# Kernel tuning notes

Measured on AMD Instinct MI355X. Metric: run time of the kernel, lower is better.

Reference implementation:

```python
import math
import jax, jax.numpy as jnp
import numpy as np
from jax import lax

# (new_dilation, init_dilation) per layer for layers=3, blocks=2, kernel_size=2
DILATIONS = [(1, 1), (2, 1), (4, 2), (1, 4), (2, 1), (4, 2)]
K = 2  # kernel_size


def dilate(x, dilation, init_dilation):
    """Faithful port of the pad+permute+view+permute trick. x: (n, c, l)."""
    n, c, l = x.shape
    f = dilation / init_dilation
    if f == 1:
        return x
    new_l = int(math.ceil(l / f) * f)
    if new_l != l:
        x = jnp.pad(x, ((0, 0), (0, 0), (new_l - l, 0)))  # pad_start=True
        l = new_l
    l_new = int(math.ceil(l * init_dilation / dilation))
    n_new = int(math.ceil(n * dilation / init_dilation))
    x = jnp.transpose(x, (1, 2, 0)).reshape(c, l_new, n_new)
    return jnp.transpose(x, (2, 0, 1))


def conv2(x, w):
    """1D conv, kernel_size=2, no bias. x:(n,i,l), w:(o,i,2) -> (n,o,l-1)."""
    return (jnp.einsum('oi,nil->nol', w[:, :, 0], x[:, :, :-1])
            + jnp.einsum('oi,nil->nol', w[:, :, 1], x[:, :, 1:]))


def conv1x1(x, w):
    return jnp.einsum('oi,nil->nol', w, x)


def maxpool3s2(x):
    return lax.reduce_window(x, -jnp.inf, lax.max, (1, 1, 3), (1, 1, 2), 'VALID')


def wavenet_logits(x, start_w, filter_w, gate_w, res_w, skip_w,
                   end1_w, end1_b, end2_w, end2_b,
                   fc_w1, fc_b1, fc_w2, fc_b2, fc_w3, fc_b3):
    h = conv1x1(x, start_w)
    skip = None
    for i, (d, idil) in enumerate(DILATIONS):
        residual = dilate(h, d, idil)
        filt = jnp.tanh(conv2(residual, filter_w[i]))
        gate = jax.nn.sigmoid(conv2(residual, gate_w[i]))
        h = filt * gate
        s = h if h.shape[2] == 1 else dilate(h, 1, d)
        s = conv1x1(s, skip_w[i])
        if skip is None:
            skip = s
        else:
            skip = s + skip[:, :, -s.shape[2]:]
        h = conv1x1(h, res_w[i]) + residual[:, :, K - 1:]
    y = jax.nn.relu(skip)                                   # (B, 256, 1272)
    y = jax.nn.relu(conv1x1(y, end1_w) + end1_b[None, :, None])
    y = maxpool3s2(y)                                       # (B, 128, 635)
    y = jax.nn.relu(conv1x1(y, end2_w) + end2_b[None, :, None])
    y = maxpool3s2(y)                                       # (B, 32, 317)
    y = y.reshape(y.shape[0], -1)                           # (B, 10144)
    # output_layer MLP (dropout = identity in eval)
    y = jax.nn.relu(y @ fc_w1.T + fc_b1)
    y = jax.nn.relu(y @ fc_w2.T + fc_b2)
    return y @ fc_w3.T + fc_b3                              # (B, num_classes)


def setup_inputs() -> dict:
    key = jax.random.key(0)
    ks = jax.random.split(key, 12)
    f32 = jnp.float32

    def w(k, shape, fan_in):
        return jax.random.normal(k, shape, f32) / np.sqrt(fan_in).astype(np.float32)

    B, Cin, L = 256, 5, 1280
    return {
        'x': jax.random.normal(ks[0], (B, Cin, L), f32),
        'start_w': w(ks[1], (32, 5), 5),
        'filter_w': w(ks[2], (6, 32, 32, 2), 64),
        'gate_w': w(ks[3], (6, 32, 32, 2), 64),
        'res_w': w(ks[4], (6, 32, 32), 32),
        'skip_w': w(ks[5], (6, 256, 32), 32),
        'end1_w': w(ks[6], (128, 256), 256), 'end1_b': jnp.zeros((128,), f32),
        'end2_w': w(ks[7], (32, 128), 128), 'end2_b': jnp.zeros((32,), f32),
        'fc_w1': w(ks[8], (1024, 10144), 10144), 'fc_b1': jnp.zeros((1024,), f32),
        'fc_w2': w(ks[9], (256, 1024), 1024), 'fc_b2': jnp.zeros((256,), f32),
        'fc_w3': w(ks[10], (2, 256), 256), 'fc_b3': jnp.zeros((2,), f32),
    }


def reference(x, start_w, filter_w, gate_w, res_w, skip_w,
              end1_w, end1_b, end2_w, end2_b,
              fc_w1, fc_b1, fc_w2, fc_b2, fc_w3, fc_b3):
    logits = wavenet_logits(x, start_w, filter_w, gate_w, res_w, skip_w,
                            end1_w, end1_b, end2_w, end2_b,
                            fc_w1, fc_b1, fc_w2, fc_b2, fc_w3, fc_b3)
    y_prob = jax.nn.softmax(logits, axis=1)
    y_hat = jnp.argmax(logits, axis=1)
    return logits, y_prob, y_hat
```

## Files before the change

### kernel.cpp

```cpp
#include <hip/hip_runtime.h>
#include <math.h>


#define MCAP 327680

typedef short v8s __attribute__((ext_vector_type(8)));
typedef float v4f __attribute__((ext_vector_type(4)));

static inline long lmax_(long a, long b) { return a > b ? a : b; }

__device__ inline unsigned short rnbf(float x) {
    unsigned u = __float_as_uint(x);
    return (unsigned short)((u + 0x7FFFu + ((u >> 16) & 1u)) >> 16);
}
__device__ inline void split2(float v, unsigned short& h, unsigned short& l) {
    h = rnbf(v);
    const float hf = __uint_as_float(((unsigned)h) << 16);
    l = rnbf(v - hf);
}
__device__ inline unsigned packsplit(float v) {
    unsigned short h, l;
    split2(v, h, l);
    return ((unsigned)l << 16) | (unsigned)h;
}
__device__ inline float unpack2f(unsigned v) {
    return __uint_as_float(v << 16) + __uint_as_float(v & 0xffff0000u);
}

__global__ __launch_bounds__(256) void k_zero(float* __restrict__ p, int n) {
    int i = blockIdx.x * 256 + threadIdx.x;
    if (i < n) p[i] = 0.f;
}

__global__ __launch_bounds__(256) void k_start(const float* __restrict__ x,
                                               const float* __restrict__ sw,
                                               unsigned* __restrict__ h0) {
    int j = blockIdx.x * 256 + threadIdx.x;
    int t = j >> 8, n = j & 255;
    float xv[5];
#pragma unroll
    for (int i = 0; i < 5; ++i) xv[i] = x[n * 6400 + i * 1280 + t];
#pragma unroll
    for (int o = 0; o < 32; ++o) {
        float acc = 0.f;
#pragma unroll
        for (int i = 0; i < 5; ++i) acc = fmaf(sw[o * 5 + i], xv[i], acc);
        h0[o * MCAP + j] = packsplit(acc);
    }
}

__global__ __launch_bounds__(256) void k_prep(const float* __restrict__ skw,
                                              const float* __restrict__ e1w,
                                              const float* __restrict__ fw,
                                              const float* __restrict__ gw,
                                              const float* __restrict__ rw,
                                              const float* __restrict__ e2w,
                                              unsigned short* __restrict__ swt_hi,
                                              unsigned short* __restrict__ swt_lo,
                                              unsigned short* __restrict__ e1t_hi,
                                              unsigned short* __restrict__ e1t_lo,
                                              unsigned short* __restrict__ wfg_hi,
                                              unsigned short* __restrict__ wfg_lo,
                                              unsigned short* __restrict__ wr_hi,
                                              unsigned short* __restrict__ wr_lo,
                                              unsigned short* __restrict__ e2s_hi,
                                              unsigned short* __restrict__ e2s_lo) {
    int idx = blockIdx.x * 256 + threadIdx.x;
    if (idx < 49152) {
        int ch = idx / 192, k = idx - ch * 192;
        int l = k >> 5, i = k & 31;
        unsigned short h, lo;
        split2(skw[l * 8192 + ch * 32 + i], h, lo);
        swt_hi[idx] = h; swt_lo[idx] = lo;
    }
    if (idx < 32768) {
        unsigned short h, lo;
        split2(e1w[idx], h, lo);
        e1t_hi[idx] = h; e1t_lo[idx] = lo;
    }
    if (idx < 24576) {
        int l = idx >> 12, r = idx & 4095;
        int row = r >> 6, k = r & 63;
        int o = row & 31, i = k & 31, tap = k >> 5;
        const float* src = (row < 32) ? fw : gw;
        unsigned short h, lo;
        split2(src[l * 2048 + o * 64 + i * 2 + tap], h, lo);
        wfg_hi[idx] = h; wfg_lo[idx] = lo;
    }
    if (idx < 12288) {
        int l = idx >> 11, r = idx & 2047;
        int o = r >> 6, k = r & 63, i = k & 31;
        unsigned short h, lo;
        split2(rw[l * 1024 + o * 32 + i], h, lo);
        wr_hi[idx] = h; wr_lo[idx] = lo;
    }
    if (idx < 4096) {
        unsigned short h, lo;
        split2(e2w[idx], h, lo);
        e2s_hi[idx] = h; e2s_lo[idx] = lo;
    }
}

__global__ __launch_bounds__(256) void k_prep_w1(const float* __restrict__ w1,
                                                 unsigned short* __restrict__ hi,
                                                 unsigned short* __restrict__ lo) {
    int idx = blockIdx.x * 256 + threadIdx.x;
    if (idx < 10387456) {
        unsigned short h, l;
        split2(w1[idx], h, l);
        hi[idx] = h; lo[idx] = l;
    }
}

__global__ __launch_bounds__(256) void k_layer_m(
    const unsigned* __restrict__ hin, const int hinBase, const int hinStride,
    unsigned* __restrict__ hout, const int houtBase, const int houtStride,
    unsigned* __restrict__ gsl, const int gStride,
    const unsigned short* __restrict__ wfg_hi, const unsigned short* __restrict__ wfg_lo,
    const unsigned short* __restrict__ wr_hi, const unsigned short* __restrict__ wr_lo,
    const int Jlo, const int NpmP, const int padN,
    const int so_, const int M0, const int M1, const int doRes)
{
    __shared__ unsigned short U[128 * 136];
    unsigned short* AT = U;
    unsigned short* GT = U;

    const int tid = threadIdx.x;
    const int j0 = Jlo + blockIdx.x * 128;

    {
        const int col = tid & 127;
        const int kg = tid >> 7;
        unsigned short* bh = &AT[col * 136 + kg * 32];
        unsigned short* bl = &AT[col * 136 + 64 + kg * 32];
        if (kg == 0 && j0 < padN) {
            uint4 z; z.x = z.y = z.z = z.w = 0u;
#pragma unroll
            for (int ch = 0; ch < 32; ch += 8) {
                *(uint4*)&bh[ch] = z;
                *(uint4*)&bl[ch] = z;
            }
        } else {
            const int off = (kg == 0) ? (j0 - padN) : (j0 + NpmP);
            const unsigned* p = hin + (off - hinBase) + col;
#pragma unroll
            for (int ch = 0; ch < 32; ch += 8) {
                alignas(16) unsigned short h8[8], l8[8];
#pragma unroll
                for (int u = 0; u < 8; ++u) {
                    const unsigned v = p[(size_t)(ch + u) * hinStride];
                    h8[u] = (unsigned short)(v & 0xffffu);
                    l8[u] = (unsigned short)(v >> 16);
                }
                *(uint4*)&bh[ch] = *(uint4*)h8;
                *(uint4*)&bl[ch] = *(uint4*)l8;
            }
        }
    }
    __syncthreads();

    const int lane = tid & 63;
    const int w    = tid >> 6;
    const int ch2  = w >> 1;
    const int mh   = w & 1;
    const int l15  = lane & 15;
    const int quad = lane >> 4;
    const int q8   = quad * 8;
    const int colb = ch2 * 64;

    v4f accf[4], accg[4];
#pragma unroll
    for (int nt = 0; nt < 4; ++nt) { accf[nt] = (v4f)(0.f); accg[nt] = (v4f)(0.f); }

#pragma unroll
    for (int kt = 0; kt < 2; ++kt) {
        const int frow = (mh * 16 + l15) * 64 + kt * 32 + q8;
        const int grow = (32 + mh * 16 + l15) * 64 + kt * 32 + q8;
        const v8s afh = *(const v8s*)&wfg_hi[frow];
        const v8s afl = *(const v8s*)&wfg_lo[frow];
        const v8s agh = *(const v8s*)&wfg_hi[grow];
        const v8s agl = *(const v8s*)&wfg_lo[grow];
#pragma unroll
        for (int nt = 0; nt < 4; ++nt) {
            const int col = colb + nt * 16 + l15;
            const v8s bh = *(const v8s*)&AT[col * 136 + kt * 32 + q8];
            const v8s bl = *(const v8s*)&AT[col * 136 + 64 + kt * 32 + q8];
            accf[nt] = __builtin_amdgcn_mfma_f32_16x16x32_bf16(afh, bh, accf[nt], 0, 0, 0);
            accf[nt] = __builtin_amdgcn_mfma_f32_16x16x32_bf16(afh, bl, accf[nt], 0, 0, 0);
            accf[nt] = __builtin_amdgcn_mfma_f32_16x16x32_bf16(afl, bh, accf[nt], 0, 0, 0);
            accg[nt] = __builtin_amdgcn_mfma_f32_16x16x32_bf16(agh, bh, accg[nt], 0, 0, 0);
            accg[nt] = __builtin_amdgcn_mfma_f32_16x16x32_bf16(agh, bl, accg[nt], 0, 0, 0);
            accg[nt] = __builtin_amdgcn_mfma_f32_16x16x32_bf16(agl, bh, accg[nt], 0, 0, 0);
        }
    }

    unsigned short gh[4][4], gl[4][4];
#pragma unroll
    for (int nt = 0; nt < 4; ++nt)
#pragma unroll
        for (int r = 0; r < 4; ++r) {
            const float f = accf[nt][r];
            const float g = accg[nt][r];
            const float th = 1.f - 2.f / (__expf(2.f * f) + 1.f);
            const float sg = 1.f / (1.f + __expf(-g));
            split2(th * sg, gh[nt][r], gl[nt][r]);
        }

    const int m0c = j0 - so_;
    if (m0c >= M0 && m0c < M1) {
#pragma unroll
        for (int nt = 0; nt < 4; ++nt)
#pragma unroll
            for (int r = 0; r < 4; ++r) {
                const int ch = mh * 16 + quad * 4 + r;
                const int m = (m0c - M0) + colb + nt * 16 + l15;
                gsl[(size_t)ch * gStride + m] =
                    ((unsigned)gl[nt][r] << 16) | (unsigned)gh[nt][r];
            }
    }

    if (doRes) {
        __syncthreads();
#pragma unroll
        for (int nt = 0; nt < 4; ++nt)
#pragma unroll
            for (int r = 0; r < 4; ++r) {
                const int ch = mh * 16 + quad * 4 + r;
                const int col = colb + nt * 16 + l15;
                GT[col * 72 + ch] = gh[nt][r];
                GT[col * 72 + 32 + ch] = gl[nt][r];
            }
        __syncthreads();

        v4f accr[4];
#pragma unroll
        for (int nt = 0; nt < 4; ++nt) accr[nt] = (v4f)(0.f);
#pragma unroll
        for (int kt = 0; kt < 2; ++kt) {
            const int row = (mh * 16 + l15) * 64 + kt * 32 + q8;
            const v8s arh = *(const v8s*)&wr_hi[row];
            const v8s arl = *(const v8s*)&wr_lo[row];
#pragma unroll
            for (int nt = 0; nt < 4; ++nt) {
                const int col = colb + nt * 16 + l15;
                const v8s b = *(const v8s*)&GT[col * 72 + kt * 32 + q8];
                accr[nt] = __builtin_amdgcn_mfma_f32_16x16x32_bf16(arh, b, accr[nt], 0, 0, 0);
                accr[nt] = __builtin_amdgcn_mfma_f32_16x16x32_bf16(arl, b, accr[nt], 0, 0, 0);
            }
        }

        const unsigned* tp = hin + (j0 + NpmP - hinBase);
#pragma unroll
        for (int nt = 0; nt < 4; ++nt)
#pragma unroll
            for (int r = 0; r < 4; ++r) {
                const int o = mh * 16 + quad * 4 + r;
                const int col = colb + nt * 16 + l15;
                const float tap1 = unpack2f(tp[(size_t)o * hinStride + col]);
                hout[(size_t)o * houtStride + (j0 - houtBase) + col] =
                    packsplit(accr[nt][r] + tap1);
            }
    }
}

__global__ __launch_bounds__(256, 2) void k_skip_end1_m(
    const unsigned* __restrict__ g,
    const unsigned short* __restrict__ swt_hi, const unsigned short* __restrict__ swt_lo,
    const unsigned short* __restrict__ e1t_hi, const unsigned short* __restrict__ e1t_lo,
    const float* __restrict__ b1, float* __restrict__ y1, const int gs)
{
    __shared__ unsigned short U[33792];
    unsigned short* gt_hi = U;
    unsigned short* gt_lo = U + 12800;
    unsigned short* st_hi = U;
    unsigned short* st_lo = U + 16896;

    const int tid  = threadIdx.x;
    const int m0   = blockIdx.x * 64;
    const int lane = tid & 63;
    const int w    = tid >> 6;
    const int l15  = lane & 15;
    const int q8   = (lane >> 4) * 8;
    const int rbase = (lane >> 4) * 4;

    {
        const int scol = tid & 63;
        const int ks0  = (tid >> 6) * 8;
        for (int kc = 0; kc < 192; kc += 32) {
            alignas(16) unsigned short h8[8], l8[8];
#pragma unroll
            for (int j = 0; j < 8; ++j) {
                const int k = kc + ks0 + j;
                const unsigned v = g[(size_t)(k >> 5) * 32 * gs + (size_t)(k & 31) * gs + m0 + scol];
                h8[j] = (unsigned short)(v & 0xffffu);
                l8[j] = (unsigned short)(v >> 16);
            }
            *(v8s*)&gt_hi[scol * 200 + kc + ks0] = *(v8s*)h8;
            *(v8s*)&gt_lo[scol * 200 + kc + ks0] = *(v8s*)l8;
        }
    }
    __syncthreads();

    v4f acc1[4][4];
#pragma unroll
    for (int a = 0; a < 4; ++a)
#pragma unroll
        for (int b = 0; b < 4; ++b) acc1[a][b] = (v4f)(0.f);

    for (int kc = 0; kc < 192; kc += 32) {
        v8s ah[4], al[4], bh[4], bl[4];
#pragma unroll
        for (int t = 0; t < 4; ++t) {
            const int row = (w * 64 + t * 16 + l15) * 192 + kc + q8;
            ah[t] = *(const v8s*)&swt_hi[row];
            al[t] = *(const v8s*)&swt_lo[row];
            const int bo = (t * 16 + l15) * 200 + kc + q8;
            bh[t] = *(const v8s*)&gt_hi[bo];
            bl[t] = *(const v8s*)&gt_lo[bo];
        }
#pragma unroll
        for (int ct = 0; ct < 4; ++ct)
#pragma unroll
            for (int nt = 0; nt < 4; ++nt) {
                acc1[ct][nt] = __builtin_amdgcn_mfma_f32_16x16x32_bf16(ah[ct], bh[nt], acc1[ct][nt], 0, 0, 0);
                acc1[ct][nt] = __builtin_amdgcn_mfma_f32_16x16x32_bf16(ah[ct], bl[nt], acc1[ct][nt], 0, 0, 0);
                acc1[ct][nt] = __builtin_amdgcn_mfma_f32_16x16x32_bf16(al[ct], bh[nt], acc1[ct][nt], 0, 0, 0);
            }
    }
    __syncthreads();

#pragma unroll
    for (int ct = 0; ct < 4; ++ct)
#pragma unroll
        for (int nt = 0; nt < 4; ++nt) {
            alignas(8) unsigned short sh[4], sl[4];
#pragma unroll
            for (int r = 0; r < 4; ++r) {
                const float v = fmaxf(acc1[ct][nt][r], 0.f);
                split2(v, sh[r], sl[r]);
            }
            const int ci  = w * 64 + ct * 16 + rbase;
            const int col = nt * 16 + l15;
            *(uint2*)&st_hi[col * 264 + ci] = *(uint2*)sh;
            *(uint2*)&st_lo[col * 264 + ci] = *(uint2*)sl;
        }
    __syncthreads();

    v4f acc2[2][4];
#pragma unroll
    for (int a = 0; a < 2; ++a)
#pragma unroll
        for (int b = 0; b < 4; ++b) acc2[a][b] = (v4f)(0.f);

    for (int kc = 0; kc < 256; kc += 32) {
        v8s ah[2], al[2], bh[4], bl[4];
#pragma unroll
        for (int t = 0; t < 2; ++t) {
            const int row = (w * 32 + t * 16 + l15) * 256 + kc + q8;
            ah[t] = *(const v8s*)&e1t_hi[row];
            al[t] = *(const v8s*)&e1t_lo[row];
        }
#pragma unroll
        for (int t = 0; t < 4; ++t) {
            const int bo = (t * 16 + l15) * 264 + kc + q8;
            bh[t] = *(const v8s*)&st_hi[bo];
            bl[t] = *(const v8s*)&st_lo[bo];
        }
#pragma unroll
        for (int ct = 0; ct < 2; ++ct)
#pragma unroll
            for (int nt = 0; nt < 4; ++nt) {
                acc2[ct][nt] = __builtin_amdgcn_mfma_f32_16x16x32_bf16(ah[ct], bh[nt], acc2[ct][nt], 0, 0, 0);
                acc2[ct][nt] = __builtin_amdgcn_mfma_f32_16x16x32_bf16(ah[ct], bl[nt], acc2[ct][nt], 0, 0, 0);
                acc2[ct][nt] = __builtin_amdgcn_mfma_f32_16x16x32_bf16(al[ct], bh[nt], acc2[ct][nt], 0, 0, 0);
            }
    }

#pragma unroll
    for (int ct = 0; ct < 2; ++ct) {
        const int cobase = w * 32 + ct * 16 + rbase;
        float bb[4];
#pragma unroll
        for (int r = 0; r < 4; ++r) bb[r] = b1[cobase + r];
#pragma unroll
        for (int nt = 0; nt < 4; ++nt) {
            const int col = m0 + nt * 16 + l15;
#pragma unroll
            for (int r = 0; r < 4; ++r)
                y1[(size_t)(cobase + r) * gs + col] = fmaxf(acc2[ct][nt][r] + bb[r], 0.f);
        }
    }
}

__global__ __launch_bounds__(256) void k_pe2_m(
    const float* __restrict__ y1c,
    const unsigned short* __restrict__ e2s_hi, const unsigned short* __restrict__ e2s_lo,
    const float* __restrict__ b2, float* __restrict__ e2c,
    const int gs, const int p1s)
{
    __shared__ unsigned short SP[2 * 64 * 136];
    unsigned short* sp_hi = SP;
    unsigned short* sp_lo = SP + 64 * 136;

    const int tid = threadIdx.x;
    const int m0 = blockIdx.x * 64;
    const int tp = m0 >> 8;
    const int nb = m0 & 255;

    {
        const int col = tid & 63;
        const int cig = tid >> 6;
        const int base = 2 * tp * 256 + nb + col;
#pragma unroll
        for (int u8 = 0; u8 < 4; ++u8) {
            alignas(16) unsigned short h8[8], l8[8];
#pragma unroll
            for (int u = 0; u < 8; ++u) {
                const int ci = cig * 32 + u8 * 8 + u;
                const float* yp = y1c + (size_t)ci * gs + base;
                const float v = fmaxf(fmaxf(yp[0], yp[256]), yp[512]);
                split2(v, h8[u], l8[u]);
            }
            *(uint4*)&sp_hi[col * 136 + cig * 32 + u8 * 8] = *(uint4*)h8;
            *(uint4*)&sp_lo[col * 136 + cig * 32 + u8 * 8] = *(uint4*)l8;
        }
    }
    __syncthreads();

    const int lane = tid & 63;
    const int w    = tid >> 6;
    const int mh   = w & 1;
    const int colh = w >> 1;
    const int l15  = lane & 15;
    const int quad = lane >> 4;
    const int q8   = quad * 8;

    v4f acc[2];
    acc[0] = (v4f)(0.f); acc[1] = (v4f)(0.f);

#pragma unroll
    for (int kc = 0; kc < 128; kc += 32) {
        const int row = (mh * 16 + l15) * 128 + kc + q8;
        const v8s ah = *(const v8s*)&e2s_hi[row];
        const v8s al = *(const v8s*)&e2s_lo[row];
#pragma unroll
        for (int nt = 0; nt < 2; ++nt) {
            const int col = colh * 32 + nt * 16 + l15;
            const v8s bh = *(const v8s*)&sp_hi[col * 136 + kc + q8];
            const v8s bl = *(const v8s*)&sp_lo[col * 136 + kc + q8];
            acc[nt] = __builtin_amdgcn_mfma_f32_16x16x32_bf16(ah, bh, acc[nt], 0, 0, 0);
            acc[nt] = __builtin_amdgcn_mfma_f32_16x16x32_bf16(ah, bl, acc[nt], 0, 0, 0);
            acc[nt] = __builtin_amdgcn_mfma_f32_16x16x32_bf16(al, bh, acc[nt], 0, 0, 0);
        }
    }

#pragma unroll
    for (int nt = 0; nt < 2; ++nt)
#pragma unroll
        for (int r = 0; r < 4; ++r) {
            const int co = mh * 16 + quad * 4 + r;
            const int col = m0 + colh * 32 + nt * 16 + l15;
            e2c[(size_t)co * p1s + col] = fmaxf(acc[nt][r] + b2[co], 0.f);
        }
}

__global__ __launch_bounds__(256) void k_pool2p(const float* __restrict__ e2c,
                                                unsigned* __restrict__ p2,
                                                const int p1s, const int A) {
    const int n = threadIdx.x, tl2 = blockIdx.x, co = blockIdx.y;
    const int base = co * p1s + tl2 * 512 + n;
    float v = fmaxf(fmaxf(e2c[base], e2c[base + 256]), e2c[base + 512]);
    p2[co * 81152 + (A + tl2) * 256 + n] = packsplit(v);
}

__global__ __launch_bounds__(256) void k_fc1_m(
    const unsigned short* __restrict__ w1s_hi, const unsigned short* __restrict__ w1s_lo,
    const unsigned* __restrict__ p2u, float* __restrict__ out)
{
    __shared__ unsigned short SB[2 * 64 * 40];
    unsigned short* sb_hi = SB;
    unsigned short* sb_lo = SB + 64 * 40;

    const int tid = threadIdx.x;
    const int o0 = blockIdx.x * 64;
    const int b0 = blockIdx.y * 64;
    const int k0 = blockIdx.z * 1280;
    const int kend = (k0 + 1280 < 10144) ? (k0 + 1280) : 10144;
    const int nch = (kend - k0) >> 5;

    const int lane = tid & 63;
    const int w    = tid >> 6;
    const int l15  = lane & 15;
    const int quad = lane >> 4;
    const int q8   = quad * 8;
    const int scol = tid & 63;
    const int kq   = tid >> 6;

    v4f acc[4];
#pragma unroll
    for (int nt = 0; nt < 4; ++nt) acc[nt] = (v4f)(0.f);

    for (int c = 0; c < nch; ++c) {
        const int kc = k0 + c * 32;
        alignas(16) unsigned short h8[8], l8[8];
#pragma unroll
        for (int j = 0; j < 8; ++j) {
            const unsigned v = p2u[(size_t)(kc + kq * 8 + j) * 256 + b0 + scol];
            h8[j] = (unsigned short)(v & 0xffffu);
            l8[j] = (unsigned short)(v >> 16);
        }
        __syncthreads();
        *(v8s*)&sb_hi[scol * 40 + kq * 8] = *(v8s*)h8;
        *(v8s*)&sb_lo[scol * 40 + kq * 8] = *(v8s*)l8;
        __syncthreads();

        const int arow = (o0 + w * 16 + l15) * 10144 + kc + q8;
        const v8s ah = *(const v8s*)&w1s_hi[arow];
        const v8s al = *(const v8s*)&w1s_lo[arow];
#pragma unroll
        for (int nt = 0; nt < 4; ++nt) {
            const v8s bh = *(const v8s*)&sb_hi[(nt * 16 + l15) * 40 + q8];
            const v8s bl = *(const v8s*)&sb_lo[(nt * 16 + l15) * 40 + q8];
            acc[nt] = __builtin_amdgcn_mfma_f32_16x16x32_bf16(ah, bh, acc[nt], 0, 0, 0);
            acc[nt] = __builtin_amdgcn_mfma_f32_16x16x32_bf16(ah, bl, acc[nt], 0, 0, 0);
            acc[nt] = __builtin_amdgcn_mfma_f32_16x16x32_bf16(al, bh, acc[nt], 0, 0, 0);
        }
    }

#pragma unroll
    for (int nt = 0; nt < 4; ++nt)
#pragma unroll
        for (int r = 0; r < 4; ++r)
            atomicAdd(&out[(size_t)(o0 + w * 16 + quad * 4 + r) * 256 + b0 + nt * 16 + l15],
                      acc[nt][r]);
}

__global__ __launch_bounds__(256) void k_gemm64(const float* __restrict__ A,
                                                const float* __restrict__ B,
                                                float* __restrict__ C,
                                                const int Ktot, const int KC) {
    __shared__ float sA[32 * 65];
    __shared__ float sB[32 * 68];

    const int tid = threadIdx.x;
    const int o0 = blockIdx.x * 64;
    const int b0 = blockIdx.y * 64;
    const int k0 = blockIdx.z * KC;

    float acc[4][4];
#pragma unroll
    for (int i = 0; i < 4; ++i)
#pragma unroll
        for (int jq = 0; jq < 4; ++jq) acc[i][jq] = 0.f;

    const int ao  = tid >> 2;
    const int ak8 = (tid & 3) * 8;
    const int bk  = tid >> 3;
    const int bb8 = (tid & 7) * 8;
    const int to4 = (tid & 15) * 4;
    const int tb4 = (tid >> 4) * 4;

    for (int kc = 0; kc < KC; kc += 32) {
        const int kcLen = (KC - kc < 32) ? (KC - kc) : 32;
        const float* ap = A + (size_t)(o0 + ao) * Ktot + k0 + kc + ak8;
#pragma unroll
        for (int i = 0; i < 8; ++i) {
            float v = (ak8 + i < kcLen) ? ap[i] : 0.f;
            sA[(ak8 + i) * 65 + ao] = v;
        }
        if (bk < kcLen) {
            const float* bp = B + (size_t)(k0 + kc + bk) * 256 + b0 + bb8;
            const float4 v0 = *(const float4*)bp;
            const float4 v1 = *(const float4*)(bp + 4);
            *(float4*)&sB[bk * 68 + bb8] = v0;
            *(float4*)&sB[bk * 68 + bb8 + 4] = v1;
        } else {
            float4 z; z.x = z.y = z.z = z.w = 0.f;
            *(float4*)&sB[bk * 68 + bb8] = z;
            *(float4*)&sB[bk * 68 + bb8 + 4] = z;
        }
        __syncthreads();

#pragma unroll 8
        for (int kk = 0; kk < 32; ++kk) {
            const float4 av = *(const float4*)&sA[kk * 65 + to4];
            const float4 bv = *(const float4*)&sB[kk * 68 + tb4];
            const float aa[4] = {av.x, av.y, av.z, av.w};
#pragma unroll
            for (int i = 0; i < 4; ++i) {
                acc[i][0] = fmaf(aa[i], bv.x, acc[i][0]);
                acc[i][1] = fmaf(aa[i], bv.y, acc[i][1]);
                acc[i][2] = fmaf(aa[i], bv.z, acc[i][2]);
                acc[i][3] = fmaf(aa[i], bv.w, acc[i][3]);
            }
        }
        __syncthreads();
    }

#pragma unroll
    for (int i = 0; i < 4; ++i)
#pragma unroll
        for (int jq = 0; jq < 4; ++jq)
            atomicAdd(&C[(size_t)(o0 + to4 + i) * 256 + b0 + tb4 + jq], acc[i][jq]);
}

__global__ __launch_bounds__(256) void k_actbias(const float* __restrict__ raw,
                                                 const float* __restrict__ bias,
                                                 float* __restrict__ out) {
    const int k = blockIdx.x, b = threadIdx.x;
    out[k * 256 + b] = fmaxf(raw[k * 256 + b] + bias[k], 0.f);
}

__global__ __launch_bounds__(256) void k_fc3(const float* __restrict__ fc2raw,
                                             const float* __restrict__ fb2,
                                             const float* __restrict__ w3,
                                             const float* __restrict__ b3,
                                             float* __restrict__ out) {
    const int b = threadIdx.x;
    float l0 = b3[0], l1 = b3[1];
    for (int k = 0; k < 256; ++k) {
        const float a = fmaxf(fc2raw[k * 256 + b] + fb2[k], 0.f);
        l0 = fmaf(w3[k], a, l0);
        l1 = fmaf(w3[256 + k], a, l1);
    }
    out[2 * b] = l0;
    out[2 * b + 1] = l1;
    const float mx = fmaxf(l0, l1);
    const float e0 = expf(l0 - mx), e1 = expf(l1 - mx);
    const float inv = 1.f / (e0 + e1);
    out[512 + 2 * b] = e0 * inv;
    out[513 + 2 * b] = e1 * inv;
    out[1024 + b] = (l1 > l0) ? 1.f : 0.f;
}

extern "C" void kernel_launch(void* const* d_in, const int* in_sizes, int n_in,
                              void* d_out, int out_size, void* d_ws, size_t ws_size,
                              hipStream_t stream) {
    const float* x        = (const float*)d_in[0];
    const float* start_w  = (const float*)d_in[1];
    const float* filter_w = (const float*)d_in[2];
    const float* gate_w   = (const float*)d_in[3];
    const float* res_w    = (const float*)d_in[4];
    const float* skip_w   = (const float*)d_in[5];
    const float* e1w      = (const float*)d_in[6];
    const float* e1b      = (const float*)d_in[7];
    const float* e2w      = (const float*)d_in[8];
    const float* e2b      = (const float*)d_in[9];
    const float* w1       = (const float*)d_in[10];
    const float* fb1      = (const float*)d_in[11];
    const float* w2       = (const float*)d_in[12];
    const float* fb2      = (const float*)d_in[13];
    const float* w3       = (const float*)d_in[14];
    const float* b3       = (const float*)d_in[15];

    float* ws = (float*)d_ws;

    const long o_h0   = 0;
    const long o_p2   = 10485760;
    const long o_fc1  = 13082624;
    const long o_fc2  = 13344768;
    const long o_wbf  = 13410304;
    const long o_wfg  = 13492224;
    const long o_wr   = 13516800;
    const long o_e2s  = 13529088;
    const long o_act1 = 13533184;
    const long o_w1s  = 13795328;
    const long o_G    = 24182784;

    long budget = (long)((double)ws_size * 0.94 / 4.0);
    int dB = 1;
    for (int d = 317; d >= 1; --d) {
        long mch = 256L * (4L * d + 3), hs = mch + 4096;
        long tot = o_G + 192L * mch + lmax_(128L * mch, 64L * hs);
        if (tot <= budget) { dB = d; break; }
    }
    int K = (317 + dB - 1) / dB;
    dB = (317 + K - 1) / K;
    const long MchA  = 256L * (4L * dB + 3);
    const long HSPAN = MchA + 4096;
    const long o_X   = o_G + 192L * MchA;
    const long P1S   = 256L * (2L * dB + 1);

    unsigned* h0 = (unsigned*)(ws + o_h0);
    unsigned* p2 = (unsigned*)(ws + o_p2);
    float* fc1r = ws + o_fc1;
    float* fc2r = ws + o_fc2;
    unsigned short* swt_hi = (unsigned short*)(ws + o_wbf);
    unsigned short* swt_lo = swt_hi + 49152;
    unsigned short* e1t_hi = swt_lo + 49152;
    unsigned short* e1t_lo = e1t_hi + 32768;
    unsigned short* wfg_hi = (unsigned short*)(ws + o_wfg);
    unsigned short* wfg_lo = wfg_hi + 24576;
    unsigned short* wr_hi  = (unsigned short*)(ws + o_wr);
    unsigned short* wr_lo  = wr_hi + 12288;
    unsigned short* e2s_hi = (unsigned short*)(ws + o_e2s);
    unsigned short* e2s_lo = e2s_hi + 4096;
    unsigned short* w1s_hi = (unsigned short*)(ws + o_w1s);
    unsigned short* w1s_lo = w1s_hi + 10387456;
    float* act1 = ws + o_act1;
    unsigned* G  = (unsigned*)(ws + o_G);
    unsigned* hA = (unsigned*)(ws + o_X);
    unsigned* hB = (unsigned*)(ws + o_X) + 32L * HSPAN;
    float* y1c  = ws + o_X;
    float* e2c  = ws + o_G;

    k_zero<<<1280, 256, 0, stream>>>(fc1r, 327680);
    k_start<<<1280, 256, 0, stream>>>(x, start_w, h0);
    k_prep<<<192, 256, 0, stream>>>(skip_w, e1w, filter_w, gate_w, res_w, e2w,
                                    swt_hi, swt_lo, e1t_hi, e1t_lo,
                                    wfg_hi, wfg_lo, wr_hi, wr_lo,
                                    e2s_hi, e2s_lo);
    k_prep_w1<<<40576, 256, 0, stream>>>(w1, w1s_hi, w1s_lo);

    const int Mc[6]   = {327424, 327168, 326656, 326400, 326144, 325632};
    const int NpmP[6] = {256, 256, 512, 256, 256, 512};
    const int pN[6]   = {0, 256, 512, 0, 256, 512};
    const int so_[6]  = {1792, 1536, 1024, 768, 512, 0};
    const int JloO[6] = {-1536, -1280, -768, -768, -512, 0};

    for (int c = 0; c < K; ++c) {
        const int A = c * dB;
        int B = A + dB; if (B > 317) B = 317;
        const int dBc = B - A;
        const int M0 = 1024 * A;
        int tmax = 4 * B + 3; if (tmax > 1272) tmax = 1272;
        const int Tt = tmax - 4 * A;
        const int M1 = M0 + 256 * Tt;

        int Jlo[6], Jhi[6];
        for (int q = 0; q < 6; ++q) {
            int lo = M0 + JloO[q]; if (lo < 0) lo = 0;
            int hi = M1 + so_[q];  if (hi > Mc[q]) hi = Mc[q];
            Jlo[q] = lo; Jhi[q] = hi;
        }

        for (int q = 0; q < 6; ++q) {
            const unsigned* hin = (q == 0) ? h0 : ((q & 1) ? hA : hB);
            const int hinBase   = (q == 0) ? 0 : Jlo[q - 1];
            const int hinStride = (q == 0) ? MCAP : (int)HSPAN;
            unsigned* hout = (q & 1) ? hB : hA;
            const int Jcnt = Jhi[q] - Jlo[q];
            k_layer_m<<<Jcnt / 128, 256, 0, stream>>>(
                hin, hinBase, hinStride, hout, Jlo[q], (int)HSPAN,
                G + (long)q * 32 * MchA, (int)MchA,
                wfg_hi + q * 4096, wfg_lo + q * 4096,
                wr_hi + q * 2048, wr_lo + q * 2048,
                Jlo[q], NpmP[q], pN[q], so_[q], M0, M1, (q < 5) ? 1 : 0);
        }

        const int Mchc = 256 * Tt;
        k_skip_end1_m<<<Mchc / 64, 256, 0, stream>>>(
            G, swt_hi, swt_lo, e1t_hi, e1t_lo, e1b, y1c, (int)MchA);
        const int T1c = 2 * dBc + 1;
        k_pe2_m<<<T1c * 4, 256, 0, stream>>>(
            y1c, e2s_hi, e2s_lo, e2b, e2c, (int)MchA, (int)P1S);
        k_pool2p<<<dim3(dBc, 32), 256, 0, stream>>>(e2c, p2, (int)P1S, A);
    }

    k_fc1_m<<<dim3(16, 4, 8), 256, 0, stream>>>(w1s_hi, w1s_lo, p2, fc1r);
    k_actbias<<<1024, 256, 0, stream>>>(fc1r, fb1, act1);
    k_gemm64<<<dim3(4, 4, 4), 256, 0, stream>>>(w2, act1, fc2r, 1024, 256);
    k_fc3<<<1, 256, 0, stream>>>(fc2r, fb2, w3, b3, (float*)d_out);
}
```

Before: 836.9 us.

## Halve shared memory in skip/end1 kernel via two-phase K staging for occupancy

The fused skip+end1 kernel now stages the gated input in two K-halves and processes the 256-channel intermediate in two 128-channel halves, cutting LDS from about 66KB to about 34KB. The end1 weights are permuted at prep time so each half's channel ordering matches the new per-wave layout. Launch bounds rise from 2 to 4 blocks per SM to exploit the freed LDS. This trades extra barriers and register pressure (acc1 plus acc2 live at once under a tighter VGPR budget) for higher occupancy.

```diff
diff --git a/kernel.cpp b/kernel.cpp
--- a/kernel.cpp
+++ b/kernel.cpp
@@ -74,8 +74,11 @@
         swt_hi[idx] = h; swt_lo[idx] = lo;
     }
     if (idx < 32768) {
+        int co = idx >> 8, kn = idx & 255;
+        int hf = kn >> 7, wv = (kn >> 5) & 3, c = (kn >> 4) & 1, r = kn & 15;
+        int ch = wv * 64 + (hf * 2 + c) * 16 + r;
         unsigned short h, lo;
-        split2(e1w[idx], h, lo);
+        split2(e1w[co * 256 + ch], h, lo);
         e1t_hi[idx] = h; e1t_lo[idx] = lo;
     }
     if (idx < 24576) {
@@ -263,17 +266,17 @@
     }
 }
 
-__global__ __launch_bounds__(256, 2) void k_skip_end1_m(
+__global__ __launch_bounds__(256, 4) void k_skip_end1_m(
     const unsigned* __restrict__ g,
     const unsigned short* __restrict__ swt_hi, const unsigned short* __restrict__ swt_lo,
     const unsigned short* __restrict__ e1t_hi, const unsigned short* __restrict__ e1t_lo,
     const float* __restrict__ b1, float* __restrict__ y1, const int gs)
 {
-    __shared__ unsigned short U[33792];
+    __shared__ unsigned short U[17408];
     unsigned short* gt_hi = U;
-    unsigned short* gt_lo = U + 12800;
+    unsigned short* gt_lo = U + 6656;
     unsigned short* st_hi = U;
-    unsigned short* st_lo = U + 16896;
+    unsigned short* st_lo = U + 8704;
 
     const int tid  = threadIdx.x;
     const int m0   = blockIdx.x * 64;
@@ -283,97 +286,105 @@
     const int q8   = (lane >> 4) * 8;
     const int rbase = (lane >> 4) * 4;
 
-    {
-        const int scol = tid & 63;
-        const int ks0  = (tid >> 6) * 8;
-        for (int kc = 0; kc < 192; kc += 32) {
+    const int scol = tid & 63;
+    const int ks0  = (tid >> 6) * 8;
+
+    v4f acc1[4][4];
+#pragma unroll
+    for (int a = 0; a < 4; ++a)
+#pragma unroll
+        for (int b = 0; b < 4; ++b) acc1[a][b] = (v4f)(0.f);
+
+#pragma unroll
+    for (int ph = 0; ph < 2; ++ph) {
+        for (int kc = 0; kc < 96; kc += 32) {
             alignas(16) unsigned short h8[8], l8[8];
 #pragma unroll
             for (int j = 0; j < 8; ++j) {
-                const int k = kc + ks0 + j;
+                const int k = ph * 96 + kc + ks0 + j;
                 const unsigned v = g[(size_t)(k >> 5) * 32 * gs + (size_t)(k & 31) * gs + m0 + scol];
                 h8[j] = (unsigned short)(v & 0xffffu);
                 l8[j] = (unsigned short)(v >> 16);
             }
-            *(v8s*)&gt_hi[scol * 200 + kc + ks0] = *(v8s*)h8;
-            *(v8s*)&gt_lo[scol * 200 + kc + ks0] = *(v8s*)l8;
-        }
-    }
-    __syncthreads();
-
-    v4f acc1[4][4];
-#pragma unroll
-    for (int a = 0; a < 4; ++a)
-#pragma unroll
-        for (int b = 0; b < 4; ++b) acc1[a][b] = (v4f)(0.f);
-
-    for (int kc = 0; kc < 192; kc += 32) {
-        v8s ah[4], al[4], bh[4], bl[4];
-#pragma unroll
-        for (int t = 0; t < 4; ++t) {
-            const int row = (w * 64 + t * 16 + l15) * 192 + kc + q8;
-            ah[t] = *(const v8s*)&swt_hi[row];
-            al[t] = *(const v8s*)&swt_lo[row];
-            const int bo = (t * 16 + l15) * 200 + kc + q8;
-            bh[t] = *(const v8s*)&gt_hi[bo];
-            bl[t] = *(const v8s*)&gt_lo[bo];
-        }
-#pragma unroll
-        for (int ct = 0; ct < 4; ++ct)
+            *(v8s*)&gt_hi[scol * 104 + kc + ks0] = *(v8s*)h8;
+            *(v8s*)&gt_lo[scol * 104 + kc + ks0] = *(v8s*)l8;
+        }
+        __syncthreads();
+
+        for (int kc = 0; kc < 96; kc += 32) {
+            v8s ah[4], al[4], bh[4], bl[4];
+#pragma unroll
+            for (int t = 0; t < 4; ++t) {
+                const int row = (w * 64 + t * 16 + l15) * 192 + ph * 96 + kc + q8;
+                ah[t] = *(const v8s*)&swt_hi[row];
+                al[t] = *(const v8s*)&swt_lo[row];
+                const int bo = (t * 16 + l15) * 104 + kc + q8;
+                bh[t] = *(const v8s*)&gt_hi[bo];
+                bl[t] = *(const v8s*)&gt_lo[bo];
+            }
+#pragma unroll
+            for (int ct = 0; ct < 4; ++ct)
+#pragma unroll
+                for (int nt = 0; nt < 4; ++nt) {
+                    acc1[ct][nt] = __builtin_amdgcn_mfma_f32_16x16x32_bf16(ah[ct], bh[nt], acc1[ct][nt], 0, 0, 0);
+                    acc1[ct][nt] = __builtin_amdgcn_mfma_f32_16x16x32_bf16(ah[ct], bl[nt], acc1[ct][nt], 0, 0, 0);
+                    acc1[ct][nt] = __builtin_amdgcn_mfma_f32_16x16x32_bf16(al[ct], bh[nt], acc1[ct][nt], 0, 0, 0);
+                }
+        }
+        __syncthreads();
+    }
+
+    v4f acc2[2][4];
+#pragma unroll
+    for (int a = 0; a < 2; ++a)
+#pragma unroll
+        for (int b = 0; b < 4; ++b) acc2[a][b] = (v4f)(0.f);
+
+#pragma unroll
+    for (int hh = 0; hh < 2; ++hh) {
+#pragma unroll
+        for (int c2 = 0; c2 < 2; ++c2) {
+            const int ct = hh * 2 + c2;
 #pragma unroll
             for (int nt = 0; nt < 4; ++nt) {
-                acc1[ct][nt] = __builtin_amdgcn_mfma_f32_16x16x32_bf16(ah[ct], bh[nt], acc1[ct][nt], 0, 0, 0);
-                acc1[ct][nt] = __builtin_amdgcn_mfma_f32_16x16x32_bf16(ah[ct], bl[nt], acc1[ct][nt], 0, 0, 0);
-                acc1[ct][nt] = __builtin_amdgcn_mfma_f32_16x16x32_bf16(al[ct], bh[nt], acc1[ct][nt], 0, 0, 0);
-            }
-    }
-    __syncthreads();
-
-#pragma unroll
-    for (int ct = 0; ct < 4; ++ct)
-#pragma unroll
-        for (int nt = 0; nt < 4; ++nt) {
-            alignas(8) unsigned short sh[4], sl[4];
-#pragma unroll
-            for (int r = 0; r < 4; ++r) {
-                const float v = fmaxf(acc1[ct][nt][r], 0.f);
-                split2(v, sh[r], sl[r]);
-            }
-            const int ci  = w * 64 + ct * 16 + rbase;
-            const int col = nt * 16 + l15;
-            *(uint2*)&st_hi[col * 264 + ci] = *(uint2*)sh;
-            *(uint2*)&st_lo[col * 264 + ci] = *(uint2*)sl;
-        }
-    __syncthreads();
-
-    v4f acc2[2][4];
-#pragma unroll
-    for (int a = 0; a < 2; ++a)
-#pragma unroll
-        for (int b = 0; b < 4; ++b) acc2[a][b] = (v4f)(0.f);
-
-    for (int kc = 0; kc < 256; kc += 32) {
-        v8s ah[2], al[2], bh[4], bl[4];
-#pragma unroll
-        for (int t = 0; t < 2; ++t) {
-            const int row = (w * 32 + t * 16 + l15) * 256 + kc + q8;
-            ah[t] = *(const v8s*)&e1t_hi[row];
-            al[t] = *(const v8s*)&e1t_lo[row];
-        }
-#pragma unroll
-        for (int t = 0; t < 4; ++t) {
-            const int bo = (t * 16 + l15) * 264 + kc + q8;
-            bh[t] = *(const v8s*)&st_hi[bo];
-            bl[t] = *(const v8s*)&st_lo[bo];
-        }
-#pragma unroll
-        for (int ct = 0; ct < 2; ++ct)
-#pragma unroll
-            for (int nt = 0; nt < 4; ++nt) {
-                acc2[ct][nt] = __builtin_amdgcn_mfma_f32_16x16x32_bf16(ah[ct], bh[nt], acc2[ct][nt], 0, 0, 0);
-                acc2[ct][nt] = __builtin_amdgcn_mfma_f32_16x16x32_bf16(ah[ct], bl[nt], acc2[ct][nt], 0, 0, 0);
-                acc2[ct][nt] = __builtin_amdgcn_mfma_f32_16x16x32_bf16(al[ct], bh[nt], acc2[ct][nt], 0, 0, 0);
-            }
+                alignas(8) unsigned short sh[4], sl[4];
+#pragma unroll
+                for (int r = 0; r < 4; ++r) {
+                    const float v = fmaxf(acc1[ct][nt][r], 0.f);
+                    split2(v, sh[r], sl[r]);
+                }
+                const int ci  = w * 32 + c2 * 16 + rbase;
+                const int col = nt * 16 + l15;
+                *(uint2*)&st_hi[col * 136 + ci] = *(uint2*)sh;
+                *(uint2*)&st_lo[col * 136 + ci] = *(uint2*)sl;
+            }
+        }
+        __syncthreads();
+
+        for (int kc = 0; kc < 128; kc += 32) {
+            v8s ah2[2], al2[2], bh2[4], bl2[4];
+#pragma unroll
+            for (int t = 0; t < 2; ++t) {
+                const int row = (w * 32 + t * 16 + l15) * 256 + hh * 128 + kc + q8;
+                ah2[t] = *(const v8s*)&e1t_hi[row];
+                al2[t] = *(const v8s*)&e1t_lo[row];
+            }
+#pragma unroll
+            for (int t = 0; t < 4; ++t) {
+                const int bo = (t * 16 + l15) * 136 + kc + q8;
+                bh2[t] = *(const v8s*)&st_hi[bo];
+                bl2[t] = *(const v8s*)&st_lo[bo];
+            }
+#pragma unroll
+            for (int ct = 0; ct < 2; ++ct)
+#pragma unroll
+                for (int nt = 0; nt < 4; ++nt) {
+                    acc2[ct][nt] = __builtin_amdgcn_mfma_f32_16x16x32_bf16(ah2[ct], bh2[nt], acc2[ct][nt], 0, 0, 0);
+                    acc2[ct][nt] = __builtin_amdgcn_mfma_f32_16x16x32_bf16(ah2[ct], bl2[nt], acc2[ct][nt], 0, 0, 0);
+                    acc2[ct][nt] = __builtin_amdgcn_mfma_f32_16x16x32_bf16(al2[ct], bh2[nt], acc2[ct][nt], 0, 0, 0);
+                }
+        }
+        if (hh == 0) __syncthreads();
     }
 
 #pragma unroll
```

Result: slower. 868.8 us (+3.8%).
